# Kernel tuning notes

Hardware: AMD Instinct MI355X
Metric: run time of the kernel (lower is better)

The kernel has to match this reference:

```python
import jax, jax.numpy as jnp
import numpy as np

NEG_SLOPE = 0.01  # torch LeakyReLU default

N_NODES = 100000
H_C = 128
N_EDGES = 1600000


def setup_inputs() -> dict:
    key = jax.random.key(0)
    k1, k2, k3, k4, k5, k6 = jax.random.split(key, 6)
    z = jax.random.normal(k1, (N_NODES, H_C), dtype=jnp.float32)
    edge_label_index = jax.random.randint(k2, (2, N_EDGES), 0, N_NODES, dtype=jnp.int64)
    # torch Linear: weight [out, in], bias [out]
    W1 = jax.random.normal(k3, (H_C, 2 * H_C), dtype=jnp.float32) / np.sqrt(2 * H_C)
    b1 = jax.random.normal(k4, (H_C,), dtype=jnp.float32) * 0.01
    W2 = jax.random.normal(k5, (1, H_C), dtype=jnp.float32) / np.sqrt(H_C)
    b2 = jax.random.normal(k6, (1,), dtype=jnp.float32) * 0.01
    return {"z": z, "edge_label_index": edge_label_index,
            "W1": W1, "b1": b1, "W2": W2, "b2": b2}


def reference(z, edge_label_index, W1, b1, W2, b2):
    row, col = edge_label_index[0], edge_label_index[1]
    # cat([z[row], z[col]], dim=1) @ W1.T == z[row] @ W1[:, :H].T + z[col] @ W1[:, H:].T
    h = z.shape[1]
    W1a, W1b = W1[:, :h], W1[:, h:]
    zc = jnp.einsum('eh,oh->eo', z[row], W1a) + jnp.einsum('eh,oh->eo', z[col], W1b) + b1
    zc = jnp.where(zc >= 0, zc, NEG_SLOPE * zc)  # LeakyReLU
    out = jnp.einsum('eh,oh->eo', zc, W2) + b2   # [E, 1]
    return out.reshape(-1)
```

## Files before the change

kernel.cpp:

```cpp
#include <hip/hip_runtime.h>
#include <hip/hip_fp16.h>

#define NN 100000
#define HC 128
#define NE 1600000

typedef float f32x4 __attribute__((ext_vector_type(4)));
typedef short bf16x8 __attribute__((ext_vector_type(8)));

__device__ __forceinline__ unsigned short f2bf(float f) {
  union { float f; unsigned u; } c; c.f = f;
  unsigned u = c.u + (0x7FFFu + ((c.u >> 16) & 1u));
  return (unsigned short)(u >> 16);
}
__device__ __forceinline__ float bf2f(unsigned short b) {
  union { unsigned u; float f; } c; c.u = ((unsigned)b) << 16;
  return c.f;
}

__global__ __launch_bounds__(256) void wprep_kernel(
    const float* __restrict__ W1, unsigned short* __restrict__ Wh,
    unsigned short* __restrict__ Wl) {
  const int idx = blockIdx.x * 256 + threadIdx.x;
  if (idx >= 256 * 128) return;
  const int o = idx >> 7;
  const int k = idx & 127;
  const float f = W1[(size_t)(o & 127) * 256 + ((o >> 7) << 7) + k];
  const unsigned short hi = f2bf(f);
  Wh[idx] = hi;
  Wl[idx] = f2bf(f - bf2f(hi));
}

__global__ __launch_bounds__(256) void precompute_uv_mfma2_kernel(
    const float* __restrict__ z, const unsigned short* __restrict__ Wh,
    const unsigned short* __restrict__ Wl, __half* __restrict__ UV) {
  const int lane = threadIdx.x & 63;
  const int wv = threadIdx.x >> 6;
  const int nb = blockIdx.x * 128 + wv * 32;
  const int lr = lane & 15;
  const int lg = lane >> 4;

  bf16x8 bh[2][4], bl[2][4];
#pragma unroll
  for (int ms = 0; ms < 2; ++ms) {
    const int node = nb + ms * 16 + lr;
    const bool ok = (node < NN);
    const float* __restrict__ zp = z + (size_t)node * HC + lg * 8;
#pragma unroll
    for (int kg = 0; kg < 4; ++kg) {
      float v[8];
      if (ok) {
        const float4 p0 = *(const float4*)(zp + kg * 32);
        const float4 p1 = *(const float4*)(zp + kg * 32 + 4);
        v[0] = p0.x; v[1] = p0.y; v[2] = p0.z; v[3] = p0.w;
        v[4] = p1.x; v[5] = p1.y; v[6] = p1.z; v[7] = p1.w;
      } else {
#pragma unroll
        for (int e = 0; e < 8; ++e) v[e] = 0.f;
      }
#pragma unroll
      for (int e = 0; e < 8; ++e) {
        const unsigned short hi = f2bf(v[e]);
        bh[ms][kg][e] = (short)hi;
        bl[ms][kg][e] = (short)f2bf(v[e] - bf2f(hi));
      }
    }
  }

#pragma unroll 1
  for (int nt = 0; nt < 16; ++nt) {
    const unsigned short* __restrict__ wph = Wh + (nt * 16 + lr) * 128 + lg * 8;
    const unsigned short* __restrict__ wpl = Wl + (nt * 16 + lr) * 128 + lg * 8;

    f32x4 acc0 = {0.f, 0.f, 0.f, 0.f};
    f32x4 acc1 = {0.f, 0.f, 0.f, 0.f};
#pragma unroll
    for (int kg = 0; kg < 4; ++kg) {
      const bf16x8 ah = *(const bf16x8*)(wph + kg * 32);
      const bf16x8 al = *(const bf16x8*)(wpl + kg * 32);
      acc0 = __builtin_amdgcn_mfma_f32_16x16x32_bf16(ah, bh[0][kg], acc0, 0, 0, 0);
      acc0 = __builtin_amdgcn_mfma_f32_16x16x32_bf16(al, bh[0][kg], acc0, 0, 0, 0);
      acc0 = __builtin_amdgcn_mfma_f32_16x16x32_bf16(ah, bl[0][kg], acc0, 0, 0, 0);
      acc1 = __builtin_amdgcn_mfma_f32_16x16x32_bf16(ah, bh[1][kg], acc1, 0, 0, 0);
      acc1 = __builtin_amdgcn_mfma_f32_16x16x32_bf16(al, bh[1][kg], acc1, 0, 0, 0);
      acc1 = __builtin_amdgcn_mfma_f32_16x16x32_bf16(ah, bl[1][kg], acc1, 0, 0, 0);
    }

    const int ob = nt * 16 + lg * 4;
    {
      const int node = nb + lr;
      if (node < NN) {
        union { uint2 u; __half2 h[2]; } pk;
        pk.h[0] = __floats2half2_rn(acc0[0], acc0[1]);
        pk.h[1] = __floats2half2_rn(acc0[2], acc0[3]);
        *(uint2*)(UV + (size_t)node * 256 + ob) = pk.u;
      }
      const int node1 = nb + 16 + lr;
      if (node1 < NN) {
        union { uint2 u; __half2 h[2]; } pk;
        pk.h[0] = __floats2half2_rn(acc1[0], acc1[1]);
        pk.h[1] = __floats2half2_rn(acc1[2], acc1[3]);
        *(uint2*)(UV + (size_t)node1 * 256 + ob) = pk.u;
      }
    }
  }
}

__global__ __launch_bounds__(256) void edge_decode_f16_kernel(
    const int* __restrict__ eidx, const __half* __restrict__ UV,
    const float* __restrict__ b1, const float* __restrict__ W2,
    const float* __restrict__ b2, float* __restrict__ out) {
  const int lane = threadIdx.x & 15;
  const int qw = (blockIdx.x * 256 + threadIdx.x) >> 4;
  const int nqw = (gridDim.x * 256) >> 4;

  const float4 b1a = ((const float4*)b1)[2 * lane];
  const float4 b1b = ((const float4*)b1)[2 * lane + 1];
  const float4 w2a = ((const float4*)W2)[2 * lane];
  const float4 w2b = ((const float4*)W2)[2 * lane + 1];
  const float bb[8] = {b1a.x, b1a.y, b1a.z, b1a.w, b1b.x, b1b.y, b1b.z, b1b.w};
  const float ww[8] = {w2a.x, w2a.y, w2a.z, w2a.w, w2b.x, w2b.y, w2b.z, w2b.w};
  const float bias2 = b2[0];

  const int* __restrict__ rows = eidx;
  const int* __restrict__ cols = eidx + NE;

#pragma unroll 2
  for (int e = qw; e < NE; e += nqw) {
    const int r = rows[e];
    const int c = cols[e];
    union { uint4 u; __half2 h[4]; } Uu, Vv;
    Uu.u = *(const uint4*)(UV + (size_t)r * 256 + lane * 8);
    Vv.u = *(const uint4*)(UV + (size_t)c * 256 + 128 + lane * 8);

    float s = 0.f;
#pragma unroll
    for (int k = 0; k < 4; ++k) {
      const float2 uf = __half22float2(Uu.h[k]);
      const float2 vf = __half22float2(Vv.h[k]);
      float t0 = uf.x + vf.x + bb[2 * k];
      t0 = (t0 >= 0.f) ? t0 : 0.01f * t0;
      s = fmaf(t0, ww[2 * k], s);
      float t1 = uf.y + vf.y + bb[2 * k + 1];
      t1 = (t1 >= 0.f) ? t1 : 0.01f * t1;
      s = fmaf(t1, ww[2 * k + 1], s);
    }

    s += __shfl_xor(s, 8);
    s += __shfl_xor(s, 4);
    s += __shfl_xor(s, 2);
    s += __shfl_xor(s, 1);
    if (lane == 0) out[e] = s + bias2;
  }
}

__global__ __launch_bounds__(64) void edge_direct_kernel(
    const float* __restrict__ z, const int* __restrict__ eidx,
    const float* __restrict__ W1, const float* __restrict__ b1,
    const float* __restrict__ W2, const float* __restrict__ b2,
    float* __restrict__ out) {
  const int lane = threadIdx.x;
  const int o0 = lane, o1 = lane + 64;
  const float w2_0 = W2[o0], w2_1 = W2[o1];
  const float b1_0 = b1[o0], b1_1 = b1[o1];
  const float bias2 = b2[0];

  for (int e = blockIdx.x; e < NE; e += gridDim.x) {
    const int r = eidx[e];
    const int c = eidx[e + NE];
    const float* __restrict__ zr = z + (size_t)r * HC;
    const float* __restrict__ zc = z + (size_t)c * HC;
    float a0 = 0.f, a1 = 0.f;
    for (int h = 0; h < HC; ++h) {
      const float zrh = zr[h], zch = zc[h];
      a0 = fmaf(zrh, W1[(size_t)o0 * 256 + h], a0);
      a0 = fmaf(zch, W1[(size_t)o0 * 256 + 128 + h], a0);
      a1 = fmaf(zrh, W1[(size_t)o1 * 256 + h], a1);
      a1 = fmaf(zch, W1[(size_t)o1 * 256 + 128 + h], a1);
    }
    a0 += b1_0; a1 += b1_1;
    a0 = (a0 >= 0.f) ? a0 : 0.01f * a0;
    a1 = (a1 >= 0.f) ? a1 : 0.01f * a1;
    float s = fmaf(a0, w2_0, a1 * w2_1);
    for (int off = 32; off >= 1; off >>= 1) s += __shfl_xor(s, off);
    if (lane == 0) out[e] = s + bias2;
  }
}

extern "C" void kernel_launch(void* const* d_in, const int* in_sizes, int n_in,
                              void* d_out, int out_size, void* d_ws, size_t ws_size,
                              hipStream_t stream) {
  const float* z  = (const float*)d_in[0];
  const int*   ei = (const int*)d_in[1];
  const float* W1 = (const float*)d_in[2];
  const float* b1 = (const float*)d_in[3];
  const float* W2 = (const float*)d_in[4];
  const float* b2 = (const float*)d_in[5];
  float* out = (float*)d_out;

  const size_t uv_bytes = (size_t)NN * 256 * sizeof(__half);
  const size_t w_bytes  = (size_t)256 * 128 * sizeof(unsigned short);

  if (ws_size >= uv_bytes + 2 * w_bytes) {
    __half* UV = (__half*)d_ws;
    unsigned short* Wh = (unsigned short*)((char*)d_ws + uv_bytes);
    unsigned short* Wl = Wh + 256 * 128;
    wprep_kernel<<<128, 256, 0, stream>>>(W1, Wh, Wl);
    precompute_uv_mfma2_kernel<<<(NN + 127) / 128, 256, 0, stream>>>(z, Wh, Wl, UV);
    edge_decode_f16_kernel<<<2048, 256, 0, stream>>>(ei, UV, b1, W2, b2, out);
  } else {
    edge_direct_kernel<<<8192, 64, 0, stream>>>(z, ei, W1, b1, W2, b2, out);
  }
}
```

Measured before the change: 187.2 us.

## Split output columns across waves in UV precompute, removing node bounds checks

The UV precompute kernel now has each block handle 32 nodes, with its four waves splitting the 256 output columns into groups of 64. Before, each wave handled 32 nodes across all 256 columns. The grid grows from 782 to 3125 blocks, giving more parallelism and a shorter serial MFMA loop per wave (4 iterations instead of 16). Because NN is divisible by 32, the node bounds checks are dropped. In exchange, each wave redundantly loads and converts the same 32 z rows, so z reads from cache are repeated four times per block.

```diff
diff --git a/kernel.cpp b/kernel.cpp
--- a/kernel.cpp
+++ b/kernel.cpp
@@ -31,12 +31,13 @@
   Wl[idx] = f2bf(f - bf2f(hi));
 }
 
-__global__ __launch_bounds__(256) void precompute_uv_mfma2_kernel(
+__global__ __launch_bounds__(256) void precompute_uv_mfma4_kernel(
     const float* __restrict__ z, const unsigned short* __restrict__ Wh,
     const unsigned short* __restrict__ Wl, __half* __restrict__ UV) {
   const int lane = threadIdx.x & 63;
   const int wv = threadIdx.x >> 6;
-  const int nb = blockIdx.x * 128 + wv * 32;
+  const int nb = blockIdx.x * 32;
+  const int og = wv * 64;
   const int lr = lane & 15;
   const int lg = lane >> 4;
 
@@ -44,20 +45,12 @@
 #pragma unroll
   for (int ms = 0; ms < 2; ++ms) {
     const int node = nb + ms * 16 + lr;
-    const bool ok = (node < NN);
     const float* __restrict__ zp = z + (size_t)node * HC + lg * 8;
 #pragma unroll
     for (int kg = 0; kg < 4; ++kg) {
-      float v[8];
-      if (ok) {
-        const float4 p0 = *(const float4*)(zp + kg * 32);
-        const float4 p1 = *(const float4*)(zp + kg * 32 + 4);
-        v[0] = p0.x; v[1] = p0.y; v[2] = p0.z; v[3] = p0.w;
-        v[4] = p1.x; v[5] = p1.y; v[6] = p1.z; v[7] = p1.w;
-      } else {
-#pragma unroll
-        for (int e = 0; e < 8; ++e) v[e] = 0.f;
-      }
+      const float4 p0 = *(const float4*)(zp + kg * 32);
+      const float4 p1 = *(const float4*)(zp + kg * 32 + 4);
+      const float v[8] = {p0.x, p0.y, p0.z, p0.w, p1.x, p1.y, p1.z, p1.w};
 #pragma unroll
       for (int e = 0; e < 8; ++e) {
         const unsigned short hi = f2bf(v[e]);
@@ -68,9 +61,10 @@
   }
 
 #pragma unroll 1
-  for (int nt = 0; nt < 16; ++nt) {
-    const unsigned short* __restrict__ wph = Wh + (nt * 16 + lr) * 128 + lg * 8;
-    const unsigned short* __restrict__ wpl = Wl + (nt * 16 + lr) * 128 + lg * 8;
+  for (int nt = 0; nt < 4; ++nt) {
+    const int orow = og + nt * 16 + lr;
+    const unsigned short* __restrict__ wph = Wh + orow * 128 + lg * 8;
+    const unsigned short* __restrict__ wpl = Wl + orow * 128 + lg * 8;
 
     f32x4 acc0 = {0.f, 0.f, 0.f, 0.f};
     f32x4 acc1 = {0.f, 0.f, 0.f, 0.f};
@@ -86,22 +80,20 @@
       acc1 = __builtin_amdgcn_mfma_f32_16x16x32_bf16(ah, bl[1][kg], acc1, 0, 0, 0);
     }
 
-    const int ob = nt * 16 + lg * 4;
+    const int ob = og + nt * 16 + lg * 4;
     {
       const int node = nb + lr;
-      if (node < NN) {
-        union { uint2 u; __half2 h[2]; } pk;
-        pk.h[0] = __floats2half2_rn(acc0[0], acc0[1]);
-        pk.h[1] = __floats2half2_rn(acc0[2], acc0[3]);
-        *(uint2*)(UV + (size_t)node * 256 + ob) = pk.u;
-      }
-      const int node1 = nb + 16 + lr;
-      if (node1 < NN) {
-        union { uint2 u; __half2 h[2]; } pk;
-        pk.h[0] = __floats2half2_rn(acc1[0], acc1[1]);
-        pk.h[1] = __floats2half2_rn(acc1[2], acc1[3]);
-        *(uint2*)(UV + (size_t)node1 * 256 + ob) = pk.u;
-      }
+      union { uint2 u; __half2 h[2]; } pk;
+      pk.h[0] = __floats2half2_rn(acc0[0], acc0[1]);
+      pk.h[1] = __floats2half2_rn(acc0[2], acc0[3]);
+      *(uint2*)(UV + (size_t)node * 256 + ob) = pk.u;
+    }
+    {
+      const int node = nb + 16 + lr;
+      union { uint2 u; __half2 h[2]; } pk;
+      pk.h[0] = __floats2half2_rn(acc1[0], acc1[1]);
+      pk.h[1] = __floats2half2_rn(acc1[2], acc1[3]);
+      *(uint2*)(UV + (size_t)node * 256 + ob) = pk.u;
     }
   }
 }
@@ -206,7 +198,7 @@
     unsigned short* Wh = (unsigned short*)((char*)d_ws + uv_bytes);
     unsigned short* Wl = Wh + 256 * 128;
     wprep_kernel<<<128, 256, 0, stream>>>(W1, Wh, Wl);
-    precompute_uv_mfma2_kernel<<<(NN + 127) / 128, 256, 0, stream>>>(z, Wh, Wl, UV);
+    precompute_uv_mfma4_kernel<<<NN / 32, 256, 0, stream>>>(z, Wh, Wl, UV);
     edge_decode_f16_kernel<<<2048, 256, 0, stream>>>(ei, UV, b1, W2, b2, out);
   } else {
     edge_direct_kernel<<<8192, 64, 0, stream>>>(z, ei, W1, b1, W2, b2, out);
```

Result: no change. 190.7 us (+1.9%).
